# Performance work log

Measured on AMD Instinct MI355X. Metric: run time of the kernel, lower is better.

Reference implementation:

```python
import jax, jax.numpy as jnp
import numpy as np

NBINS = 64
EPS = 1e-10
SIGMA = 1.0 / (NBINS - 1)


def setup_inputs() -> dict:
    key = jax.random.key(0)
    k1, k2 = jax.random.split(key)
    pred = jax.random.normal(k1, (8, 1, 512, 512), dtype=jnp.float32)
    target = jax.random.normal(k2, (8, 1, 512, 512), dtype=jnp.float32)
    return {"pred": pred, "target": target}


def _normalize(x):
    # per-sample min-max normalization to [0,1]
    B = x.shape[0]
    xf = x.reshape(B, -1)
    x_min = xf.min(axis=1, keepdims=True)
    x_max = xf.max(axis=1, keepdims=True)
    return (xf - x_min) / (x_max - x_min + EPS)  # (B, Npix)


def reference(pred, target):
    B = pred.shape[0]
    Npix = pred.shape[-2] * pred.shape[-1]
    centers = jnp.linspace(0.0, 1.0, NBINS, dtype=jnp.float32)  # (nbins,)

    pred_flat = _normalize(pred)      # (B, Npix)
    tgt_flat = _normalize(target)     # (B, Npix)

    inv2s2 = 1.0 / (2.0 * SIGMA * SIGMA)
    # Gaussian soft-binning weights: (B, Npix, nbins)
    w_pred = jnp.exp(-(pred_flat[:, :, None] - centers) ** 2 * inv2s2)
    w_tgt = jnp.exp(-(tgt_flat[:, :, None] - centers) ** 2 * inv2s2)

    # joint histogram via batched contraction over pixels: (B, nbins, nbins)
    p_xy = jnp.einsum('bni,bnj->bij', w_pred, w_tgt) / float(Npix)
    p_x = p_xy.sum(axis=2)  # (B, nbins)
    p_y = p_xy.sum(axis=1)  # (B, nbins)

    px_py = p_x[:, :, None] * p_y[:, None, :]
    ratio = (p_xy + EPS) / (px_py + EPS)
    mi = (p_xy * jnp.log(ratio)).sum(axis=(1, 2))  # (B,)
    return -mi.mean()
```

## Files before the change

kernel.cpp:

```cpp
#include <hip/hip_runtime.h>
#include <stdint.h>

#define NPIX  (512 * 512)
#define NB    8
#define NCH   8
#define CHPX  (NPIX / NCH)
#define FB    128
#define MPW   161
#define HDR_FLOATS 1024

typedef __attribute__((ext_vector_type(4))) unsigned uint4v;
typedef __attribute__((ext_vector_type(4))) float    float4v;

__device__ constexpr float WK[33] = {
  1.2664166e-14f, 6.1019365e-13f, 2.2897490e-11f, 6.6915858e-10f,
  1.5229979e-08f, 2.6995785e-07f, 3.7266532e-06f, 4.0065297e-05f,
  3.3546263e-04f, 2.1874911e-03f, 1.1108997e-02f, 4.3936934e-02f,
  1.3533528e-01f, 3.2465247e-01f, 6.0653066e-01f, 8.8249690e-01f,
  1.0f,
  8.8249690e-01f, 6.0653066e-01f, 3.2465247e-01f, 1.3533528e-01f,
  4.3936934e-02f, 1.1108997e-02f, 2.1874911e-03f, 3.3546263e-04f,
  4.0065297e-05f, 3.7266532e-06f, 2.6995785e-07f, 1.5229979e-08f,
  6.6915858e-10f, 2.2897490e-11f, 6.1019365e-13f, 1.2664166e-14f
};

__global__ __launch_bounds__(1024) void minmax_kernel(const float* __restrict__ pred,
                                                      const float* __restrict__ tgt,
                                                      float2* __restrict__ mm,
                                                      unsigned* __restrict__ cnt) {
  __shared__ float smin[16], smax[16];
  const int tid = threadIdx.x, lane = tid & 63, wave = tid >> 6;
  if (blockIdx.x == 0 && tid < 12) cnt[tid] = 0u;
  const int pair = blockIdx.x >> 4, sub = blockIdx.x & 15;
  const float* src = pair < 8 ? pred + (size_t)pair * NPIX
                              : tgt  + (size_t)(pair - 8) * NPIX;
  const float4v* s4 = (const float4v*)src + sub * 4096;
  float vmin = 3.0e38f, vmax = -3.0e38f;
  #pragma unroll
  for (int k = 0; k < 4; ++k) {
    float4v v = s4[k * 1024 + tid];
    vmin = fminf(vmin, fminf(fminf(v[0], v[1]), fminf(v[2], v[3])));
    vmax = fmaxf(vmax, fmaxf(fmaxf(v[0], v[1]), fmaxf(v[2], v[3])));
  }
  #pragma unroll
  for (int off = 32; off; off >>= 1) {
    vmin = fminf(vmin, __shfl_xor(vmin, off));
    vmax = fmaxf(vmax, __shfl_xor(vmax, off));
  }
  if (lane == 0) { smin[wave] = vmin; smax[wave] = vmax; }
  __syncthreads();
  if (tid == 0) {
    float m = smin[0], M = smax[0];
    #pragma unroll
    for (int w = 1; w < 16; ++w) { m = fminf(m, smin[w]); M = fmaxf(M, smax[w]); }
    mm[blockIdx.x] = (float2){m, M};
  }
}

__global__ __launch_bounds__(1024) void hist_tail_kernel(const float* __restrict__ pred,
                                                         const float* __restrict__ tgt,
                                                         const float2* __restrict__ mm,
                                                         unsigned* __restrict__ part,
                                                         float2* __restrict__ fineF,
                                                         unsigned* __restrict__ cnt,
                                                         float* __restrict__ mi,
                                                         float* __restrict__ out) {
  __shared__ float S[14608];
  __shared__ unsigned s_last;
  unsigned* H = (unsigned*)S;
  const int tid = threadIdx.x, lane = tid & 63, wave = tid >> 6;
  const int b = blockIdx.x >> 3, c = blockIdx.x & 7;

  float pmin = 3.0e38f, pmax = -3.0e38f, tmin = 3.0e38f, tmax = -3.0e38f;
  #pragma unroll
  for (int s2 = 0; s2 < 16; ++s2) {
    float2 a = mm[b * 16 + s2], d = mm[(8 + b) * 16 + s2];
    pmin = fminf(pmin, a.x); pmax = fmaxf(pmax, a.y);
    tmin = fminf(tmin, d.x); tmax = fmaxf(tmax, d.y);
  }
  const float sp = 126.0f / (pmax - pmin + 1e-10f), op = -pmin * sp + 0.5f;
  const float st = 126.0f / (tmax - tmin + 1e-10f), ot = -tmin * st + 0.5f;

  ((uint4v*)H)[tid]        = (uint4v){0u, 0u, 0u, 0u};
  ((uint4v*)H)[1024 + tid] = (uint4v){0u, 0u, 0u, 0u};
  __syncthreads();

  const float4v* p4 = (const float4v*)(pred + (size_t)b * NPIX + (size_t)c * CHPX);
  const float4v* t4 = (const float4v*)(tgt  + (size_t)b * NPIX + (size_t)c * CHPX);
  #pragma unroll
  for (int it = 0; it < 8; ++it) {
    float4v vp = p4[it * 1024 + tid];
    float4v vt = t4[it * 1024 + tid];
    #pragma unroll
    for (int j = 0; j < 4; ++j) {
      int fp = (int)(vp[j] * sp + op);
      int ft = (int)(vt[j] * st + ot);
      int w  = (fp << 6) | (ft >> 1);
      atomicAdd(&H[w ^ ((fp & 7) << 2)], 1u << ((ft & 1) << 4));
    }
  }
  __syncthreads();

  {
    uint4v* dst = (uint4v*)(part + ((size_t)blockIdx.x << 13));
    #pragma unroll
    for (int j = 0; j < 2; ++j) {
      int g = j * 1024 + tid;
      dst[g] = ((uint4v*)H)[g ^ ((g >> 4) & 7)];
    }
  }
  __syncthreads();
  if (tid == 0) {
    __threadfence();
    unsigned old = atomicAdd(&cnt[b], 1u);
    s_last = (old == NCH - 1) ? 1u : 0u;
    if (s_last) __threadfence();
  }
  __syncthreads();
  if (!s_last) return;

  {
    const unsigned* src = part + ((size_t)b << 16);
    float2* f2 = fineF + (size_t)b * 8192;
    #pragma unroll
    for (int q = 0; q < 8; ++q) {
      int w = q * 1024 + tid;
      unsigned lo = 0, hi = 0;
      #pragma unroll
      for (int cc = 0; cc < 8; ++cc) {
        unsigned v = src[((size_t)cc << 13) + w];
        lo += v & 0xFFFFu; hi += v >> 16;
      }
      float2 o; o.x = (float)lo; o.y = (float)hi;
      f2[w] = o;
    }
    if (tid == 0) atomicExch(&cnt[b], 0u);
  }
  __syncthreads();

  const float* fineG = (const float*)(fineF + (size_t)b * 8192);
  {
    const int ft = tid & 127, r = tid >> 7;
    const float* fb = fineG + ft;
    float v[47];
    #pragma unroll
    for (int t = 0; t < 47; ++t) {
      int fp = 16 * r - 16 + t;
      v[t] = ((unsigned)fp < 128u) ? fb[fp << 7] : 0.0f;
    }
    float acc[8];
    #pragma unroll
    for (int d = 0; d < 8; ++d) {
      float a = 0.0f;
      #pragma unroll
      for (int k = 0; k < 33; ++k) a += WK[k] * v[2 * d + k];
      acc[d] = a;
    }
    #pragma unroll
    for (int d = 0; d < 8; ++d)
      S[(8 * r + d) * MPW + ft + 16] = acc[d];
    #pragma unroll
    for (int ii = 0; ii < 3; ++ii) {
      int idx = ii * 1024 + tid;
      if (idx < 64 * 33) {
        int rr = idx / 33, cc = idx % 33;
        int col = cc < 16 ? cc : cc + 128;
        S[rr * MPW + col] = 0.0f;
      }
    }
  }
  __syncthreads();

  const int i = tid & 63, js = (tid >> 6) << 2;
  {
    float v[39];
    #pragma unroll
    for (int t = 0; t < 39; ++t) v[t] = S[i * MPW + 2 * js + t];
    float acc[4] = {0.0f, 0.0f, 0.0f, 0.0f};
    #pragma unroll
    for (int d = 0; d < 4; ++d)
      #pragma unroll
      for (int k = 0; k < 33; ++k) acc[d] += WK[k] * v[2 * d + k];
    const float invN = 1.0f / (float)NPIX;
    #pragma unroll
    for (int d = 0; d < 4; ++d) S[10304 + i * 65 + js + d] = acc[d] * invN;
  }
  __syncthreads();

  {
    const int l16 = lane & 15, sub16 = lane >> 4;
    int row = 4 * wave + sub16;
    float s = 0.0f;
    #pragma unroll
    for (int k = 0; k < 4; ++k) s += S[10304 + row * 65 + l16 * 4 + k];
    #pragma unroll
    for (int off = 8; off; off >>= 1) s += __shfl_xor(s, off);
    if (l16 == 0) S[14464 + row] = s;
    float t2 = 0.0f;
    #pragma unroll
    for (int k = 0; k < 4; ++k) t2 += S[10304 + (l16 * 4 + k) * 65 + row];
    #pragma unroll
    for (int off = 8; off; off >>= 1) t2 += __shfl_xor(t2, off);
    if (l16 == 0) S[14528 + row] = t2;
  }
  __syncthreads();

  float a = 0.0f;
  #pragma unroll
  for (int r = 0; r < 4; ++r) {
    int e = r * 1024 + tid;
    int ii = e >> 6, jj = e & 63;
    float pv = S[10304 + ii * 65 + jj];
    float d = S[14464 + ii] * S[14528 + jj] + 1e-10f;
    a += pv * __logf((pv + 1e-10f) / d);
  }
  #pragma unroll
  for (int off = 32; off; off >>= 1) a += __shfl_xor(a, off);
  if (lane == 0) S[14592 + wave] = a;
  __syncthreads();

  if (tid == 0) {
    float s = 0.0f;
    #pragma unroll
    for (int w = 0; w < 16; ++w) s += S[14592 + w];
    atomicExch(&mi[b], s);
    __threadfence();
    unsigned prev = atomicAdd(&cnt[8], 1u);
    if (prev == NB - 1) {
      __threadfence();
      float tot = 0.0f;
      #pragma unroll
      for (int k = 0; k < NB; ++k) tot += atomicAdd(&mi[k], 0.0f);
      out[0] = -(tot * (1.0f / NB));
      atomicExch(&cnt[8], 0u);
    }
  }
}

extern "C" void kernel_launch(void* const* d_in, const int* in_sizes, int n_in,
                              void* d_out, int out_size, void* d_ws, size_t ws_size,
                              hipStream_t stream) {
  const float* pred = (const float*)d_in[0];
  const float* tgt  = (const float*)d_in[1];
  float*    out  = (float*)d_out;
  float*    wsf  = (float*)d_ws;
  float2*   mm   = (float2*)d_ws;
  float*    mi   = wsf + 512;
  unsigned* cnt  = (unsigned*)(wsf + 520);
  unsigned* part = (unsigned*)(wsf + HDR_FLOATS);
  float2*   fineF = (float2*)(wsf + HDR_FLOATS + (size_t)NB * NCH * 8192);

  minmax_kernel   <<<256,      1024, 0, stream>>>(pred, tgt, mm, cnt);
  hist_tail_kernel<<<NB * NCH, 1024, 0, stream>>>(pred, tgt, mm, part, fineF, cnt, mi, out);
}
```

Baseline: 33.58 us.

## Split histogram into 32 chunks per sample with two-level merge

Raises the number of histogram chunks per sample from 8 to 32, so the histogram kernel launches 256 blocks instead of 64 and fills more CUs on the GPU. Partial histograms are merged in two stages. The last of each group of 8 chunks merges that group's partials, and the last of the 4 groups then sums the group results and runs the tail computation. This adds global traffic for partial histograms and an extra counter and fence stage, and each block does more fixed work (clearing and writing its histogram) relative to the pixels it processes.

```diff
diff --git a/kernel.cpp b/kernel.cpp
--- a/kernel.cpp
+++ b/kernel.cpp
@@ -3,7 +3,7 @@
 
 #define NPIX  (512 * 512)
 #define NB    8
-#define NCH   8
+#define NCH   32
 #define CHPX  (NPIX / NCH)
 #define FB    128
 #define MPW   161
@@ -30,7 +30,7 @@
                                                       unsigned* __restrict__ cnt) {
   __shared__ float smin[16], smax[16];
   const int tid = threadIdx.x, lane = tid & 63, wave = tid >> 6;
-  if (blockIdx.x == 0 && tid < 12) cnt[tid] = 0u;
+  if (blockIdx.x == 0 && tid < 41) cnt[tid] = 0u;
   const int pair = blockIdx.x >> 4, sub = blockIdx.x & 15;
   const float* src = pair < 8 ? pred + (size_t)pair * NPIX
                               : tgt  + (size_t)(pair - 8) * NPIX;
@@ -61,7 +61,8 @@
                                                          const float* __restrict__ tgt,
                                                          const float2* __restrict__ mm,
                                                          unsigned* __restrict__ part,
-                                                         float2* __restrict__ fineF,
+                                                         unsigned* __restrict__ merged,
+                                                         float* __restrict__ fineF,
                                                          unsigned* __restrict__ cnt,
                                                          float* __restrict__ mi,
                                                          float* __restrict__ out) {
@@ -69,7 +70,7 @@
   __shared__ unsigned s_last;
   unsigned* H = (unsigned*)S;
   const int tid = threadIdx.x, lane = tid & 63, wave = tid >> 6;
-  const int b = blockIdx.x >> 3, c = blockIdx.x & 7;
+  const int blk = blockIdx.x, b = blk >> 5, c = blk & 31;
 
   float pmin = 3.0e38f, pmax = -3.0e38f, tmin = 3.0e38f, tmax = -3.0e38f;
   #pragma unroll
@@ -88,7 +89,7 @@
   const float4v* p4 = (const float4v*)(pred + (size_t)b * NPIX + (size_t)c * CHPX);
   const float4v* t4 = (const float4v*)(tgt  + (size_t)b * NPIX + (size_t)c * CHPX);
   #pragma unroll
-  for (int it = 0; it < 8; ++it) {
+  for (int it = 0; it < 2; ++it) {
     float4v vp = p4[it * 1024 + tid];
     float4v vt = t4[it * 1024 + tid];
     #pragma unroll
@@ -102,7 +103,7 @@
   __syncthreads();
 
   {
-    uint4v* dst = (uint4v*)(part + ((size_t)blockIdx.x << 13));
+    uint4v* dst = (uint4v*)(part + ((size_t)blk << 13));
     #pragma unroll
     for (int j = 0; j < 2; ++j) {
       int g = j * 1024 + tid;
@@ -110,35 +111,58 @@
     }
   }
   __syncthreads();
+  const int g = c >> 3;
   if (tid == 0) {
     __threadfence();
-    unsigned old = atomicAdd(&cnt[b], 1u);
-    s_last = (old == NCH - 1) ? 1u : 0u;
-    if (s_last) __threadfence();
+    unsigned old = atomicAdd(&cnt[(b << 2) | g], 1u);
+    unsigned last = (old == 7u) ? 1u : 0u;
+    if (last) { atomicExch(&cnt[(b << 2) | g], 0u); __threadfence(); }
+    s_last = last;
   }
   __syncthreads();
   if (!s_last) return;
 
   {
-    const unsigned* src = part + ((size_t)b << 16);
-    float2* f2 = fineF + (size_t)b * 8192;
-    #pragma unroll
-    for (int q = 0; q < 8; ++q) {
-      int w = q * 1024 + tid;
+    const unsigned* src = part + ((size_t)(b * 32 + g * 8) << 13);
+    unsigned* mg = merged + ((size_t)((b << 2) | g) << 14);
+    #pragma unroll
+    for (int k = 0; k < 8; ++k) {
+      int w = k * 1024 + tid;
       unsigned lo = 0, hi = 0;
       #pragma unroll
       for (int cc = 0; cc < 8; ++cc) {
         unsigned v = src[((size_t)cc << 13) + w];
         lo += v & 0xFFFFu; hi += v >> 16;
       }
-      float2 o; o.x = (float)lo; o.y = (float)hi;
-      f2[w] = o;
-    }
-    if (tid == 0) atomicExch(&cnt[b], 0u);
-  }
-  __syncthreads();
-
-  const float* fineG = (const float*)(fineF + (size_t)b * 8192);
+      mg[2 * w]     = lo;
+      mg[2 * w + 1] = hi;
+    }
+  }
+  __syncthreads();
+  if (tid == 0) {
+    __threadfence();
+    unsigned old = atomicAdd(&cnt[32 + b], 1u);
+    unsigned last = (old == 3u) ? 1u : 0u;
+    if (last) { atomicExch(&cnt[32 + b], 0u); __threadfence(); }
+    s_last = last;
+  }
+  __syncthreads();
+  if (!s_last) return;
+
+  {
+    const unsigned* m0 = merged + ((size_t)(b << 2) << 14);
+    float* fo = fineF + (size_t)b * 16384;
+    #pragma unroll
+    for (int k = 0; k < 16; ++k) {
+      int cell = k * 1024 + tid;
+      unsigned s = m0[cell] + m0[(1 << 14) + cell]
+                 + m0[(2 << 14) + cell] + m0[(3 << 14) + cell];
+      fo[cell] = (float)s;
+    }
+  }
+  __syncthreads();
+
+  const float* fineG = fineF + (size_t)b * 16384;
   {
     const int ft = tid & 127, r = tid >> 7;
     const float* fb = fineG + ft;
@@ -225,14 +249,14 @@
     for (int w = 0; w < 16; ++w) s += S[14592 + w];
     atomicExch(&mi[b], s);
     __threadfence();
-    unsigned prev = atomicAdd(&cnt[8], 1u);
+    unsigned prev = atomicAdd(&cnt[40], 1u);
     if (prev == NB - 1) {
       __threadfence();
       float tot = 0.0f;
       #pragma unroll
       for (int k = 0; k < NB; ++k) tot += atomicAdd(&mi[k], 0.0f);
       out[0] = -(tot * (1.0f / NB));
-      atomicExch(&cnt[8], 0u);
+      atomicExch(&cnt[40], 0u);
     }
   }
 }
@@ -248,8 +272,10 @@
   float*    mi   = wsf + 512;
   unsigned* cnt  = (unsigned*)(wsf + 520);
   unsigned* part = (unsigned*)(wsf + HDR_FLOATS);
-  float2*   fineF = (float2*)(wsf + HDR_FLOATS + (size_t)NB * NCH * 8192);
-
-  minmax_kernel   <<<256,      1024, 0, stream>>>(pred, tgt, mm, cnt);
-  hist_tail_kernel<<<NB * NCH, 1024, 0, stream>>>(pred, tgt, mm, part, fineF, cnt, mi, out);
+  unsigned* merged = part + ((size_t)256 << 13);
+  float*    fineF  = (float*)(merged + ((size_t)32 << 14));
+
+  minmax_kernel   <<<256, 1024, 0, stream>>>(pred, tgt, mm, cnt);
+  hist_tail_kernel<<<256, 1024, 0, stream>>>(pred, tgt, mm, part, merged, fineF,
+                                             cnt, mi, out);
 }
```

Result: slower. 46.84 us (+39.5%).
